# Kernel tuning notes

Measured on AMD Instinct MI355X. Metric: run time of the kernel, lower is better.

The kernel has to match this reference:

```python
import jax, jax.numpy as jnp
import numpy as np

DIM = 1024
HEADS = 16
DIM_HEAD = 64


def setup_inputs() -> dict:
    key = jax.random.key(0)
    k1, k2 = jax.random.split(key)
    x = jax.random.normal(k1, (2, 2048, DIM), dtype=jnp.float32)
    # to_qkv: Linear(dim, 3*heads*dim_head, bias=False); torch weight is [out,in],
    # we store the transposed [in,out] form for x @ W.
    W_qkv = jax.random.normal(k2, (DIM, 3 * HEADS * DIM_HEAD), dtype=jnp.float32) * (DIM ** -0.5)
    return {"x": x, "W_qkv": W_qkv}


def reference(x, W_qkv):
    b, n, _ = x.shape
    h, d = HEADS, DIM_HEAD
    scale = d ** -0.5
    qkv = x @ W_qkv                              # [b, n, 3*h*d]
    q, k, v = jnp.split(qkv, 3, axis=-1)
    # 'b n (h d) -> b h n d'
    q = q.reshape(b, n, h, d).transpose(0, 2, 1, 3)
    k = k.reshape(b, n, h, d).transpose(0, 2, 1, 3)
    v = v.reshape(b, n, h, d).transpose(0, 2, 1, 3)
    dots = jnp.einsum('bhnd,bhmd->bhnm', q, k) * scale
    attn = jax.nn.softmax(dots, axis=-1)
    out = jnp.einsum('bhnm,bhmd->bhnd', attn, v)
    out = out.transpose(0, 2, 1, 3).reshape(b, n, h * d)  # 'b h n d -> b n (h d)'
    return out + x  # residual (to_out is never applied in the source forward)
```

## Files before the change

kernel.cpp:

```cpp
#include <hip/hip_runtime.h>

#define DIM   1024
#define NQKV  3072
#define SEQ   2048
#define HEADS 16
#define DHEAD 64
#define M_TOT 4096

typedef __bf16 bf16;
typedef __bf16 bf16x8 __attribute__((ext_vector_type(8)));
typedef float  f32x4  __attribute__((ext_vector_type(4)));

typedef const __attribute__((address_space(1))) unsigned int gu32;
typedef __attribute__((address_space(3))) unsigned int su32;

static __device__ __forceinline__ unsigned short f2b(float f) {
    bf16 h = (bf16)f;
    return __builtin_bit_cast(unsigned short, h);
}

#define CAST_BLOCKS (M_TOT * DIM / (256 * 4))
#define TR_NB (NQKV / 64)
__global__ void prep_kernel(const float* __restrict__ x,
                            unsigned short* __restrict__ xb,
                            const float* __restrict__ W,
                            unsigned short* __restrict__ Wt) {
    __shared__ float tile[64][65];
    const int id  = blockIdx.x;
    const int tid = threadIdx.x;
    if (id < CAST_BLOCKS) {
        int i = (id * 256 + tid) * 4;
        float4 v = *(const float4*)(x + i);
        ushort4 o;
        o.x = f2b(v.x); o.y = f2b(v.y); o.z = f2b(v.z); o.w = f2b(v.w);
        *(ushort4*)(xb + i) = o;
    } else {
        int t  = id - CAST_BLOCKS;
        int nb = t % TR_NB;
        int kb = t / TR_NB;
        #pragma unroll
        for (int p = 0; p < 4; p++) {
            int kl = p * 16 + (tid >> 4);
            int nl = (tid & 15) * 4;
            float4 v = *(const float4*)&W[(size_t)(kb * 64 + kl) * NQKV + nb * 64 + nl];
            tile[nl + 0][kl] = v.x;
            tile[nl + 1][kl] = v.y;
            tile[nl + 2][kl] = v.z;
            tile[nl + 3][kl] = v.w;
        }
        __syncthreads();
        #pragma unroll
        for (int p = 0; p < 2; p++) {
            int nl = p * 32 + (tid >> 3);
            int k8 = (tid & 7) * 8;
            int n  = nb * 64 + nl;
            float s = (n < 1024) ? 0.18033688f : 1.0f;
            float4 a = *(const float4*)&tile[nl][k8];
            float4 b = *(const float4*)&tile[nl][k8 + 4];
            ushort4 o0, o1;
            o0.x = f2b(a.x * s); o0.y = f2b(a.y * s); o0.z = f2b(a.z * s); o0.w = f2b(a.w * s);
            o1.x = f2b(b.x * s); o1.y = f2b(b.y * s); o1.z = f2b(b.z * s); o1.w = f2b(b.w * s);
            uint4 pk;
            pk.x = ((unsigned)o0.y << 16) | o0.x;
            pk.y = ((unsigned)o0.w << 16) | o0.z;
            pk.z = ((unsigned)o1.y << 16) | o1.x;
            pk.w = ((unsigned)o1.w << 16) | o1.z;
            *(uint4*)&Wt[(size_t)n * DIM + kb * 64 + k8] = pk;
        }
    }
}

#define LDC 136
__global__ __launch_bounds__(256) void qkv_gemm_kernel(
    const unsigned short* __restrict__ A,
    const unsigned short* __restrict__ Bt,
    unsigned short* __restrict__ Qw,
    unsigned short* __restrict__ Kw,
    unsigned short* __restrict__ Vtw)
{
    __shared__ __align__(16) unsigned char smem[65536];
    unsigned short* Cs = (unsigned short*)smem;

    const int tid  = threadIdx.x;
    const int m0   = blockIdx.y * 128;
    const int n0   = blockIdx.x * 128;
    const int w    = tid >> 6;
    const int lane = tid & 63;
    const int l16  = lane & 15;
    const int quad = lane >> 4;
    const int wm   = (w >> 1) * 64;
    const int wn   = (w & 1) * 64;
    const int srow = lane >> 3;
    const int scol = ((lane & 7) ^ srow) * 8;
    const int xa   = l16 & 7;

    f32x4 acc[4][4];
    const f32x4 fzero = {0.f, 0.f, 0.f, 0.f};
    for (int i = 0; i < 4; i++)
        for (int j = 0; j < 4; j++) acc[i][j] = fzero;

    const unsigned short* Ag = A  + (size_t)(m0 + w * 32 + srow) * DIM + scol;
    const unsigned short* Bg = Bt + (size_t)(n0 + w * 32 + srow) * DIM + scol;

    {
        unsigned short* As0 = (unsigned short*)smem;
        unsigned short* Bs0 = (unsigned short*)(smem + 16384);
        #pragma unroll
        for (int j = 0; j < 4; j++) {
            __builtin_amdgcn_global_load_lds((gu32*)(Ag + (size_t)j * 8 * DIM),
                                             (su32*)&As0[(w * 32 + j * 8) * 64], 16, 0, 0);
            __builtin_amdgcn_global_load_lds((gu32*)(Bg + (size_t)j * 8 * DIM),
                                             (su32*)&Bs0[(w * 32 + j * 8) * 64], 16, 0, 0);
        }
    }
    __syncthreads();

    for (int ki = 0; ki < 16; ki++) {
        const int cur = ki & 1, nxt = cur ^ 1;
        if (ki < 15) {
            const int kt = (ki + 1) * 64;
            unsigned short* Asn = (unsigned short*)(smem + nxt * 32768);
            unsigned short* Bsn = (unsigned short*)(smem + nxt * 32768 + 16384);
            #pragma unroll
            for (int j = 0; j < 4; j++) {
                __builtin_amdgcn_global_load_lds((gu32*)(Ag + kt + (size_t)j * 8 * DIM),
                                                 (su32*)&Asn[(w * 32 + j * 8) * 64], 16, 0, 0);
                __builtin_amdgcn_global_load_lds((gu32*)(Bg + kt + (size_t)j * 8 * DIM),
                                                 (su32*)&Bsn[(w * 32 + j * 8) * 64], 16, 0, 0);
            }
        }
        const unsigned short* As = (const unsigned short*)(smem + cur * 32768);
        const unsigned short* Bs = (const unsigned short*)(smem + cur * 32768 + 16384);
        #pragma unroll
        for (int s = 0; s < 2; s++) {
            const int col = ((s * 4 + quad) ^ xa) * 8;
            bf16x8 af[4], bfr[4];
            #pragma unroll
            for (int i = 0; i < 4; i++) {
                af[i]  = *(const bf16x8*)(&As[(wm + i * 16 + l16) * 64 + col]);
                bfr[i] = *(const bf16x8*)(&Bs[(wn + i * 16 + l16) * 64 + col]);
            }
            #pragma unroll
            for (int i = 0; i < 4; i++)
                #pragma unroll
                for (int j = 0; j < 4; j++)
                    acc[i][j] = __builtin_amdgcn_mfma_f32_16x16x32_bf16(af[i], bfr[j], acc[i][j], 0, 0, 0);
        }
        __syncthreads();
    }

    const int part = n0 >> 10;
    const int h0   = (n0 & 1023) >> 6;
    const int b    = m0 >> 11;
    const int np0  = m0 & 2047;

    if (part < 2) {
        #pragma unroll
        for (int i = 0; i < 4; i++)
            #pragma unroll
            for (int j = 0; j < 4; j++)
                #pragma unroll
                for (int r = 0; r < 4; r++)
                    Cs[(wm + i * 16 + quad * 4 + r) * LDC + wn + j * 16 + l16] = f2b(acc[i][j][r]);
        __syncthreads();
        unsigned short* dst = (part == 0) ? Qw : Kw;
        #pragma unroll
        for (int pass = 0; pass < 8; pass++) {
            int mi = pass * 16 + (tid >> 4);
            int ci = (tid & 15) * 8;
            uint4 v = *(const uint4*)&Cs[mi * LDC + ci];
            int bh = b * HEADS + h0 + (ci >> 6);
            *(uint4*)&dst[((size_t)bh * SEQ + np0 + mi) * DHEAD + (ci & 63)] = v;
        }
    } else {
        #pragma unroll
        for (int i = 0; i < 4; i++)
            #pragma unroll
            for (int j = 0; j < 4; j++) {
                ushort4 pk;
                pk.x = f2b(acc[i][j][0]); pk.y = f2b(acc[i][j][1]);
                pk.z = f2b(acc[i][j][2]); pk.w = f2b(acc[i][j][3]);
                *(ushort4*)&Cs[(wn + j * 16 + l16) * LDC + wm + i * 16 + quad * 4] = pk;
            }
        __syncthreads();
        #pragma unroll
        for (int pass = 0; pass < 8; pass++) {
            int ci = pass * 16 + (tid >> 4);
            int mi = (tid & 15) * 8;
            uint4 v = *(const uint4*)&Cs[ci * LDC + mi];
            int bh = b * HEADS + h0 + (ci >> 6);
            *(uint4*)&Vtw[((size_t)bh * DHEAD + (ci & 63)) * SEQ + np0 + mi] = v;
        }
    }
}

__global__ __launch_bounds__(512, 2) void attn_kernel(
    const unsigned short* __restrict__ Qw,
    const unsigned short* __restrict__ Kw,
    const unsigned short* __restrict__ Vtw,
    const float* __restrict__ x,
    float* __restrict__ out)
{
    __shared__ __align__(16) unsigned char smem[65536];
    unsigned short* base = (unsigned short*)smem;
    float* scratch = (float*)smem;

    const int id  = blockIdx.x;
    const int qt  = id >> 5;
    const int bh  = ((id & 7) << 2) | ((id >> 3) & 3);
    const int tid = threadIdx.x;
    const int w   = tid >> 6, lane = tid & 63;
    const int l16 = lane & 15, quad = lane >> 4;
    const int g   = w & 3;
    const int p   = w >> 2;
    const int xq  = l16 & 7;

    const unsigned short* Qb = Qw + ((size_t)bh * SEQ + qt * 256 + g * 64 + l16) * DHEAD;
    bf16x8 qf[4][2];
    #pragma unroll
    for (int qh = 0; qh < 4; qh++) {
        qf[qh][0] = *(const bf16x8*)(Qb + qh * 16 * DHEAD + quad * 8);
        qf[qh][1] = *(const bf16x8*)(Qb + qh * 16 * DHEAD + 32 + quad * 8);
    }

    bf16x8 ones;
    #pragma unroll
    for (int j = 0; j < 8; j++) ones[j] = (bf16)1.0f;

    f32x4 o[4][4], dsum[4];
    const f32x4 fzero = {0.f, 0.f, 0.f, 0.f};
    #pragma unroll
    for (int qh = 0; qh < 4; qh++) {
        #pragma unroll
        for (int d = 0; d < 4; d++) o[qh][d] = fzero;
        dsum[qh] = fzero;
    }

    const unsigned short* Kg = Kw  + (size_t)bh * SEQ * DHEAD;
    const unsigned short* Vg = Vtw + (size_t)bh * DHEAD * SEQ;

    const int sl   = lane >> 3;
    const int c16s = (lane & 7) ^ sl;
    const int pr   = 8 * w + sl;
    const int rlog = ((pr >> 2) & 3) * 8 + ((pr >> 4) & 1) * 4 + (pr & 3) + (pr & 32);
    const size_t koff = (size_t)rlog * DHEAD + c16s * 8;
    const size_t voff = (size_t)pr * SEQ + c16s * 8;

    __builtin_amdgcn_global_load_lds((gu32*)(Kg + koff), (su32*)(base + w * 512), 16, 0, 0);
    __builtin_amdgcn_global_load_lds((gu32*)(Vg + voff), (su32*)(base + 4096 + w * 512), 16, 0, 0);
    __syncthreads();

    for (int t = 0; t < 32; t++) {
        const int cur = t & 1, nxt = cur ^ 1;
        if (t + 1 < 32) {
            const size_t kb = (size_t)((t + 1) * 64) * DHEAD;
            const int kv = (t + 1) * 64;
            __builtin_amdgcn_global_load_lds((gu32*)(Kg + kb + koff),
                                             (su32*)(base + nxt * 8192 + w * 512), 16, 0, 0);
            __builtin_amdgcn_global_load_lds((gu32*)(Vg + voff + kv),
                                             (su32*)(base + nxt * 8192 + 4096 + w * 512), 16, 0, 0);
        }

        const unsigned short* Kb = base + cur * 8192;
        const unsigned short* Vb = base + cur * 8192 + 4096;

        f32x4 sacc[4][2];
        #pragma unroll
        for (int qh = 0; qh < 4; qh++)
            #pragma unroll
            for (int ki = 0; ki < 2; ki++) sacc[qh][ki] = fzero;
        #pragma unroll
        for (int s = 0; s < 2; s++) {
            const int col = ((s * 4 + quad) ^ xq) * 8;
            #pragma unroll
            for (int ki = 0; ki < 2; ki++) {
                bf16x8 kf = *(const bf16x8*)(&Kb[(p * 32 + ki * 16 + l16) * 64 + col]);
                #pragma unroll
                for (int qh = 0; qh < 4; qh++)
                    sacc[qh][ki] = __builtin_amdgcn_mfma_f32_16x16x32_bf16(kf, qf[qh][s], sacc[qh][ki], 0, 0, 0);
            }
        }

        bf16x8 pf[4];
        #pragma unroll
        for (int qh = 0; qh < 4; qh++)
            #pragma unroll
            for (int ki = 0; ki < 2; ki++)
                #pragma unroll
                for (int r = 0; r < 4; r++)
                    pf[qh][ki * 4 + r] = (bf16)__builtin_amdgcn_exp2f(sacc[qh][ki][r]);

        const int colv = ((p * 4 + quad) ^ xq) * 8;
        #pragma unroll
        for (int qh = 0; qh < 4; qh++)
            dsum[qh] = __builtin_amdgcn_mfma_f32_16x16x32_bf16(pf[qh], ones, dsum[qh], 0, 0, 0);
        #pragma unroll
        for (int d = 0; d < 4; d++) {
            bf16x8 vf = *(const bf16x8*)(&Vb[(d * 16 + l16) * 64 + colv]);
            #pragma unroll
            for (int qh = 0; qh < 4; qh++)
                o[qh][d] = __builtin_amdgcn_mfma_f32_16x16x32_bf16(pf[qh], vf, o[qh][d], 0, 0, 0);
        }
        __syncthreads();
    }

    #pragma unroll
    for (int ch = 0; ch < 2; ch++) {
        if (ch) __syncthreads();
        if (p == 1) {
            float* sc = scratch + ((size_t)(g * 64 + lane)) * 40;
            #pragma unroll
            for (int q2 = 0; q2 < 2; q2++) {
                int qh = ch * 2 + q2;
                #pragma unroll
                for (int di = 0; di < 4; di++)
                    *(f32x4*)(sc + q2 * 20 + di * 4) = o[qh][di];
                *(f32x4*)(sc + q2 * 20 + 16) = dsum[qh];
            }
        }
        __syncthreads();
        if (p == 0) {
            float* sc = scratch + ((size_t)(g * 64 + lane)) * 40;
            #pragma unroll
            for (int q2 = 0; q2 < 2; q2++) {
                int qh = ch * 2 + q2;
                #pragma unroll
                for (int di = 0; di < 4; di++)
                    o[qh][di] += *(const f32x4*)(sc + q2 * 20 + di * 4);
                dsum[qh] += *(const f32x4*)(sc + q2 * 20 + 16);
            }
        }
    }

    if (p == 0) {
        const int b = bh >> 4, h = bh & 15;
        #pragma unroll
        for (int qh = 0; qh < 4; qh++) {
            float lr[4];
            #pragma unroll
            for (int r = 0; r < 4; r++) lr[r] = __builtin_amdgcn_rcpf(dsum[qh][r]);
            #pragma unroll
            for (int di = 0; di < 4; di++)
                #pragma unroll
                for (int r = 0; r < 4; r++) {
                    int np  = qt * 256 + g * 64 + qh * 16 + quad * 4 + r;
                    int col = h * 64 + di * 16 + l16;
                    size_t gidx = ((size_t)(b * SEQ + np)) * DIM + col;
                    out[gidx] = o[qh][di][r] * lr[r] + x[gidx];
                }
        }
    }
}

extern "C" void kernel_launch(void* const* d_in, const int* in_sizes, int n_in,
                              void* d_out, int out_size, void* d_ws, size_t ws_size,
                              hipStream_t stream) {
    const float* x  = (const float*)d_in[0];
    const float* Wq = (const float*)d_in[1];
    float* out = (float*)d_out;

    unsigned short* xb = (unsigned short*)d_ws;
    unsigned short* Wt = xb + (size_t)M_TOT * DIM;
    unsigned short* Qw = Wt + (size_t)NQKV * DIM;
    unsigned short* Kw = Qw + (size_t)32 * SEQ * DHEAD;
    unsigned short* Vt = Kw + (size_t)32 * SEQ * DHEAD;

    prep_kernel<<<CAST_BLOCKS + TR_NB * (DIM / 64), 256, 0, stream>>>(x, xb, Wq, Wt);
    qkv_gemm_kernel<<<dim3(NQKV / 128, M_TOT / 128), 256, 0, stream>>>(xb, Wt, Qw, Kw, Vt);
    attn_kernel<<<(SEQ / 256) * 32, 512, 0, stream>>>(Qw, Kw, Vt, x, out);
}
```

Baseline: 149.6 us.

## Give each wave private double-buffered K/V LDS tiles and drop per-iteration barriers

Each of the 8 waves now loads its own copy of the K and V slices it needs (its 32-key half) into a private double-buffered LDS region. Readiness is tracked with `s_waitcnt vmcnt`, so the `__syncthreads` inside the KV loop goes away. This is meant to remove block-wide barrier stalls between the load and compute phases. In exchange, LDS use doubles to 128KB, which likely allows only one block per CU. Waves sharing the same half now fetch identical data, so global/L2 traffic rises about fourfold, and the V tile is read without the XOR swizzle, which risks bank conflicts.

```diff
diff --git a/kernel.cpp b/kernel.cpp
--- a/kernel.cpp
+++ b/kernel.cpp
@@ -201,7 +201,7 @@
     const float* __restrict__ x,
     float* __restrict__ out)
 {
-    __shared__ __align__(16) unsigned char smem[65536];
+    __shared__ __align__(16) unsigned char smem[131072];
     unsigned short* base = (unsigned short*)smem;
     float* scratch = (float*)smem;
 
@@ -236,33 +236,49 @@
         dsum[qh] = fzero;
     }
 
-    const unsigned short* Kg = Kw  + (size_t)bh * SEQ * DHEAD;
-    const unsigned short* Vg = Vtw + (size_t)bh * DHEAD * SEQ;
-
-    const int sl   = lane >> 3;
-    const int c16s = (lane & 7) ^ sl;
-    const int pr   = 8 * w + sl;
-    const int rlog = ((pr >> 2) & 3) * 8 + ((pr >> 4) & 1) * 4 + (pr & 3) + (pr & 32);
-    const size_t koff = (size_t)rlog * DHEAD + c16s * 8;
-    const size_t voff = (size_t)pr * SEQ + c16s * 8;
-
-    __builtin_amdgcn_global_load_lds((gu32*)(Kg + koff), (su32*)(base + w * 512), 16, 0, 0);
-    __builtin_amdgcn_global_load_lds((gu32*)(Vg + voff), (su32*)(base + 4096 + w * 512), 16, 0, 0);
-    __syncthreads();
+    const int l8 = lane & 7, sl = lane >> 3;
+    const int vrow = lane >> 2, v16 = lane & 3;
+    const int slotK = (l8 ^ sl) * 8;
+    int koff[4];
+    #pragma unroll
+    for (int i = 0; i < 4; i++) {
+        int rlog = (((2 * i + (sl >> 2)) & 3) * 8) + ((i >> 1) * 4) + (sl & 3);
+        koff[i] = rlog * DHEAD + slotK;
+    }
+
+    const unsigned short* Kg = Kw  + ((size_t)bh * SEQ + p * 32) * DHEAD;
+    const unsigned short* Vg = Vtw + (size_t)bh * DHEAD * SEQ + p * 32;
+    unsigned short* Kd0 = base + w * 8192;
+
+    #pragma unroll
+    for (int i = 0; i < 4; i++) {
+        __builtin_amdgcn_global_load_lds((gu32*)(Kg + koff[i]),
+                                         (su32*)(Kd0 + i * 512), 16, 0, 0);
+        __builtin_amdgcn_global_load_lds((gu32*)(Vg + (size_t)(i * 16 + vrow) * SEQ + v16 * 8),
+                                         (su32*)(Kd0 + 2048 + i * 512), 16, 0, 0);
+    }
 
     for (int t = 0; t < 32; t++) {
         const int cur = t & 1, nxt = cur ^ 1;
         if (t + 1 < 32) {
-            const size_t kb = (size_t)((t + 1) * 64) * DHEAD;
-            const int kv = (t + 1) * 64;
-            __builtin_amdgcn_global_load_lds((gu32*)(Kg + kb + koff),
-                                             (su32*)(base + nxt * 8192 + w * 512), 16, 0, 0);
-            __builtin_amdgcn_global_load_lds((gu32*)(Vg + voff + kv),
-                                             (su32*)(base + nxt * 8192 + 4096 + w * 512), 16, 0, 0);
-        }
-
-        const unsigned short* Kb = base + cur * 8192;
-        const unsigned short* Vb = base + cur * 8192 + 4096;
+            const unsigned short* Kt = Kg + (size_t)((t + 1) * 64) * DHEAD;
+            const unsigned short* Vt = Vg + (t + 1) * 64;
+            unsigned short* Kd = base + w * 8192 + nxt * 4096;
+            #pragma unroll
+            for (int i = 0; i < 4; i++) {
+                __builtin_amdgcn_global_load_lds((gu32*)(Kt + koff[i]),
+                                                 (su32*)(Kd + i * 512), 16, 0, 0);
+                __builtin_amdgcn_global_load_lds((gu32*)(Vt + (size_t)(i * 16 + vrow) * SEQ + v16 * 8),
+                                                 (su32*)(Kd + 2048 + i * 512), 16, 0, 0);
+            }
+            asm volatile("s_waitcnt vmcnt(8)" ::: "memory");
+        } else {
+            asm volatile("s_waitcnt vmcnt(0)" ::: "memory");
+        }
+        __builtin_amdgcn_sched_barrier(0);
+
+        const unsigned short* Kb = base + w * 8192 + cur * 4096;
+        const unsigned short* Vb = Kb + 2048;
 
         f32x4 sacc[4][2];
         #pragma unroll
@@ -274,7 +290,7 @@
             const int col = ((s * 4 + quad) ^ xq) * 8;
             #pragma unroll
             for (int ki = 0; ki < 2; ki++) {
-                bf16x8 kf = *(const bf16x8*)(&Kb[(p * 32 + ki * 16 + l16) * 64 + col]);
+                bf16x8 kf = *(const bf16x8*)(&Kb[(ki * 16 + l16) * 64 + col]);
                 #pragma unroll
                 for (int qh = 0; qh < 4; qh++)
                     sacc[qh][ki] = __builtin_amdgcn_mfma_f32_16x16x32_bf16(kf, qf[qh][s], sacc[qh][ki], 0, 0, 0);
@@ -290,20 +306,19 @@
                 for (int r = 0; r < 4; r++)
                     pf[qh][ki * 4 + r] = (bf16)__builtin_amdgcn_exp2f(sacc[qh][ki][r]);
 
-        const int colv = ((p * 4 + quad) ^ xq) * 8;
         #pragma unroll
         for (int qh = 0; qh < 4; qh++)
             dsum[qh] = __builtin_amdgcn_mfma_f32_16x16x32_bf16(pf[qh], ones, dsum[qh], 0, 0, 0);
         #pragma unroll
         for (int d = 0; d < 4; d++) {
-            bf16x8 vf = *(const bf16x8*)(&Vb[(d * 16 + l16) * 64 + colv]);
+            bf16x8 vf = *(const bf16x8*)(&Vb[(d * 16 + l16) * 32 + quad * 8]);
             #pragma unroll
             for (int qh = 0; qh < 4; qh++)
                 o[qh][d] = __builtin_amdgcn_mfma_f32_16x16x32_bf16(pf[qh], vf, o[qh][d], 0, 0, 0);
         }
-        __syncthreads();
-    }
-
+    }
+
+    __syncthreads();
     #pragma unroll
     for (int ch = 0; ch < 2; ch++) {
         if (ch) __syncthreads();
```

After: 151.2 us. About the same (+1.1%).

## Enlarge QKV GEMM tile to 256x128, single-buffer LDS, two blocks per CU

Applied to the files above, without the earlier changes.

The QKV projection GEMM tile grows from 128x128 to 256x128, so each wave computes a 128x64 sub-tile with 8x4 accumulators, which raises operand reuse and halves the grid. LDS drops to 48KB with a single buffer, and launch bounds request two blocks per CU so occupancy can hide load latency instead of explicit double buffering. The epilogue now stages the output in two halves through LDS with extra barriers. Risks are exposed global load latency without prefetch, higher register pressure from 128 accumulator floats, and fewer blocks (384) to spread across the CUs.

```diff
diff --git a/kernel.cpp b/kernel.cpp
--- a/kernel.cpp
+++ b/kernel.cpp
@@ -71,125 +71,130 @@
 }
 
 #define LDC 136
-__global__ __launch_bounds__(256) void qkv_gemm_kernel(
+__global__ __launch_bounds__(256, 2) void qkv_gemm_kernel(
     const unsigned short* __restrict__ A,
     const unsigned short* __restrict__ Bt,
     unsigned short* __restrict__ Qw,
     unsigned short* __restrict__ Kw,
     unsigned short* __restrict__ Vtw)
 {
-    __shared__ __align__(16) unsigned char smem[65536];
+    __shared__ __align__(16) unsigned char smem[49152];
+    unsigned short* As = (unsigned short*)smem;
+    unsigned short* Bs = (unsigned short*)(smem + 32768);
     unsigned short* Cs = (unsigned short*)smem;
 
     const int tid  = threadIdx.x;
-    const int m0   = blockIdx.y * 128;
+    const int m0   = blockIdx.y * 256;
     const int n0   = blockIdx.x * 128;
     const int w    = tid >> 6;
     const int lane = tid & 63;
     const int l16  = lane & 15;
     const int quad = lane >> 4;
-    const int wm   = (w >> 1) * 64;
+    const int wm   = (w >> 1) * 128;
     const int wn   = (w & 1) * 64;
     const int srow = lane >> 3;
     const int scol = ((lane & 7) ^ srow) * 8;
     const int xa   = l16 & 7;
 
-    f32x4 acc[4][4];
+    f32x4 acc[8][4];
     const f32x4 fzero = {0.f, 0.f, 0.f, 0.f};
-    for (int i = 0; i < 4; i++)
+    #pragma unroll
+    for (int i = 0; i < 8; i++)
+        #pragma unroll
         for (int j = 0; j < 4; j++) acc[i][j] = fzero;
 
-    const unsigned short* Ag = A  + (size_t)(m0 + w * 32 + srow) * DIM + scol;
+    const unsigned short* Ag = A  + (size_t)(m0 + w * 64 + srow) * DIM + scol;
     const unsigned short* Bg = Bt + (size_t)(n0 + w * 32 + srow) * DIM + scol;
 
-    {
-        unsigned short* As0 = (unsigned short*)smem;
-        unsigned short* Bs0 = (unsigned short*)(smem + 16384);
-        #pragma unroll
-        for (int j = 0; j < 4; j++) {
-            __builtin_amdgcn_global_load_lds((gu32*)(Ag + (size_t)j * 8 * DIM),
-                                             (su32*)&As0[(w * 32 + j * 8) * 64], 16, 0, 0);
-            __builtin_amdgcn_global_load_lds((gu32*)(Bg + (size_t)j * 8 * DIM),
-                                             (su32*)&Bs0[(w * 32 + j * 8) * 64], 16, 0, 0);
-        }
-    }
-    __syncthreads();
-
     for (int ki = 0; ki < 16; ki++) {
-        const int cur = ki & 1, nxt = cur ^ 1;
-        if (ki < 15) {
-            const int kt = (ki + 1) * 64;
-            unsigned short* Asn = (unsigned short*)(smem + nxt * 32768);
-            unsigned short* Bsn = (unsigned short*)(smem + nxt * 32768 + 16384);
-            #pragma unroll
-            for (int j = 0; j < 4; j++) {
-                __builtin_amdgcn_global_load_lds((gu32*)(Ag + kt + (size_t)j * 8 * DIM),
-                                                 (su32*)&Asn[(w * 32 + j * 8) * 64], 16, 0, 0);
-                __builtin_amdgcn_global_load_lds((gu32*)(Bg + kt + (size_t)j * 8 * DIM),
-                                                 (su32*)&Bsn[(w * 32 + j * 8) * 64], 16, 0, 0);
-            }
-        }
-        const unsigned short* As = (const unsigned short*)(smem + cur * 32768);
-        const unsigned short* Bs = (const unsigned short*)(smem + cur * 32768 + 16384);
+        const int kt = ki * 64;
+        if (ki > 0) __syncthreads();
+        #pragma unroll
+        for (int j = 0; j < 8; j++)
+            __builtin_amdgcn_global_load_lds((gu32*)(Ag + kt + (size_t)j * 8 * DIM),
+                                             (su32*)&As[(w * 64 + j * 8) * 64], 16, 0, 0);
+        #pragma unroll
+        for (int j = 0; j < 4; j++)
+            __builtin_amdgcn_global_load_lds((gu32*)(Bg + kt + (size_t)j * 8 * DIM),
+                                             (su32*)&Bs[(w * 32 + j * 8) * 64], 16, 0, 0);
+        __syncthreads();
+
         #pragma unroll
         for (int s = 0; s < 2; s++) {
             const int col = ((s * 4 + quad) ^ xa) * 8;
-            bf16x8 af[4], bfr[4];
-            #pragma unroll
-            for (int i = 0; i < 4; i++) {
+            bf16x8 af[8], bfr[4];
+            #pragma unroll
+            for (int i = 0; i < 8; i++)
                 af[i]  = *(const bf16x8*)(&As[(wm + i * 16 + l16) * 64 + col]);
-                bfr[i] = *(const bf16x8*)(&Bs[(wn + i * 16 + l16) * 64 + col]);
-            }
-            #pragma unroll
-            for (int i = 0; i < 4; i++)
+            #pragma unroll
+            for (int j = 0; j < 4; j++)
+                bfr[j] = *(const bf16x8*)(&Bs[(wn + j * 16 + l16) * 64 + col]);
+            #pragma unroll
+            for (int i = 0; i < 8; i++)
                 #pragma unroll
                 for (int j = 0; j < 4; j++)
                     acc[i][j] = __builtin_amdgcn_mfma_f32_16x16x32_bf16(af[i], bfr[j], acc[i][j], 0, 0, 0);
         }
-        __syncthreads();
-    }
+    }
+    __syncthreads();
 
     const int part = n0 >> 10;
     const int h0   = (n0 & 1023) >> 6;
-    const int b    = m0 >> 11;
-    const int np0  = m0 & 2047;
 
     if (part < 2) {
-        #pragma unroll
-        for (int i = 0; i < 4; i++)
-            #pragma unroll
-            for (int j = 0; j < 4; j++)
-                #pragma unroll
-                for (int r = 0; r < 4; r++)
-                    Cs[(wm + i * 16 + quad * 4 + r) * LDC + wn + j * 16 + l16] = f2b(acc[i][j][r]);
-        __syncthreads();
         unsigned short* dst = (part == 0) ? Qw : Kw;
         #pragma unroll
-        for (int pass = 0; pass < 8; pass++) {
-            int mi = pass * 16 + (tid >> 4);
-            int ci = (tid & 15) * 8;
-            uint4 v = *(const uint4*)&Cs[mi * LDC + ci];
-            int bh = b * HEADS + h0 + (ci >> 6);
-            *(uint4*)&dst[((size_t)bh * SEQ + np0 + mi) * DHEAD + (ci & 63)] = v;
+        for (int half = 0; half < 2; half++) {
+            if (half) __syncthreads();
+            if ((w >> 1) == half) {
+                #pragma unroll
+                for (int i = 0; i < 8; i++)
+                    #pragma unroll
+                    for (int j = 0; j < 4; j++)
+                        #pragma unroll
+                        for (int r = 0; r < 4; r++)
+                            Cs[(i * 16 + quad * 4 + r) * LDC + wn + j * 16 + l16] = f2b(acc[i][j][r]);
+            }
+            __syncthreads();
+            const int mg  = m0 + half * 128;
+            const int b   = mg >> 11;
+            const int npb = mg & 2047;
+            #pragma unroll
+            for (int pass = 0; pass < 8; pass++) {
+                int mi = pass * 16 + (tid >> 4);
+                int ci = (tid & 15) * 8;
+                uint4 v = *(const uint4*)&Cs[mi * LDC + ci];
+                int bh = b * HEADS + h0 + (ci >> 6);
+                *(uint4*)&dst[((size_t)bh * SEQ + npb + mi) * DHEAD + (ci & 63)] = v;
+            }
         }
     } else {
         #pragma unroll
-        for (int i = 0; i < 4; i++)
-            #pragma unroll
-            for (int j = 0; j < 4; j++) {
-                ushort4 pk;
-                pk.x = f2b(acc[i][j][0]); pk.y = f2b(acc[i][j][1]);
-                pk.z = f2b(acc[i][j][2]); pk.w = f2b(acc[i][j][3]);
-                *(ushort4*)&Cs[(wn + j * 16 + l16) * LDC + wm + i * 16 + quad * 4] = pk;
-            }
-        __syncthreads();
-        #pragma unroll
-        for (int pass = 0; pass < 8; pass++) {
-            int ci = pass * 16 + (tid >> 4);
-            int mi = (tid & 15) * 8;
-            uint4 v = *(const uint4*)&Cs[ci * LDC + mi];
-            int bh = b * HEADS + h0 + (ci >> 6);
-            *(uint4*)&Vtw[((size_t)bh * DHEAD + (ci & 63)) * SEQ + np0 + mi] = v;
+        for (int half = 0; half < 2; half++) {
+            if (half) __syncthreads();
+            if ((w >> 1) == half) {
+                #pragma unroll
+                for (int i = 0; i < 8; i++)
+                    #pragma unroll
+                    for (int j = 0; j < 4; j++) {
+                        ushort4 pk;
+                        pk.x = f2b(acc[i][j][0]); pk.y = f2b(acc[i][j][1]);
+                        pk.z = f2b(acc[i][j][2]); pk.w = f2b(acc[i][j][3]);
+                        *(ushort4*)&Cs[(wn + j * 16 + l16) * LDC + i * 16 + quad * 4] = pk;
+                    }
+            }
+            __syncthreads();
+            const int mg  = m0 + half * 128;
+            const int b   = mg >> 11;
+            const int npb = mg & 2047;
+            #pragma unroll
+            for (int pass = 0; pass < 8; pass++) {
+                int ci = pass * 16 + (tid >> 4);
+                int mi = (tid & 15) * 8;
+                uint4 v = *(const uint4*)&Cs[ci * LDC + mi];
+                int bh = b * HEADS + h0 + (ci >> 6);
+                *(uint4*)&Vtw[((size_t)bh * DHEAD + (ci & 63)) * SEQ + npb + mi] = v;
+            }
         }
     }
 }
@@ -366,6 +371,6 @@
     unsigned short* Vt = Kw + (size_t)32 * SEQ * DHEAD;
 
     prep_kernel<<<CAST_BLOCKS + TR_NB * (DIM / 64), 256, 0, stream>>>(x, xb, Wq, Wt);
-    qkv_gemm_kernel<<<dim3(NQKV / 128, M_TOT / 128), 256, 0, stream>>>(xb, Wt, Qw, Kw, Vt);
+    qkv_gemm_kernel<<<dim3(NQKV / 128, M_TOT / 256), 256, 0, stream>>>(xb, Wt, Qw, Kw, Vt);
     attn_kernel<<<(SEQ / 256) * 32, 512, 0, stream>>>(Qw, Kw, Vt, x, out);
 }
```

Measured after the change: 145.8 us. 2.5% less time.
